# Optimization experiments

Hardware: AMD Instinct MI355X
Metric: run time of the kernel (lower is better)

The kernel has to match this reference:

```python
import jax, jax.numpy as jnp
import numpy as np

B, T, V, H, C = 512, 512, 64, 128, 4


def setup_inputs() -> dict:
    key = jax.random.key(0)
    ks = jax.random.split(key, 32)
    s = 0.05  # weight scale
    inp = {
        'x': jax.random.normal(ks[0], (B, T, V), jnp.float32),
        'd': jax.random.uniform(ks[1], (B, T, 1), jnp.float32),
        'm1': (jax.random.uniform(ks[2], (B, T, V)) < 0.5).astype(jnp.float32),
        'h0_1': 0.1 * jax.random.normal(ks[3], (B, H), jnp.float32),
        'h0_2': 0.1 * jax.random.normal(ks[4], (B, H), jnp.float32),
        'h0_3': 0.1 * jax.random.normal(ks[5], (B, H), jnp.float32),
        'W_ih1': s * jax.random.normal(ks[6], (3 * H, V), jnp.float32),
        'W_hh1': s * jax.random.normal(ks[7], (3 * H, H), jnp.float32),
        'b_ih1': jnp.zeros((3 * H,), jnp.float32),
        'b_hh1': jnp.zeros((3 * H,), jnp.float32),
        'W_ih2': s * jax.random.normal(ks[8], (3 * H, H), jnp.float32),
        'W_hh2': s * jax.random.normal(ks[9], (3 * H, H), jnp.float32),
        'b_ih2': jnp.zeros((3 * H,), jnp.float32),
        'b_hh2': jnp.zeros((3 * H,), jnp.float32),
        'W_ih3': s * jax.random.normal(ks[10], (3 * H, H), jnp.float32),
        'W_hh3': s * jax.random.normal(ks[11], (3 * H, H), jnp.float32),
        'b_ih3': jnp.zeros((3 * H,), jnp.float32),
        'b_hh3': jnp.zeros((3 * H,), jnp.float32),
        'W_out': s * jax.random.normal(ks[12], (C, H), jnp.float32),
        'b_out': jax.random.uniform(ks[13], (C,), jnp.float32),
        'W_dx': s * jax.random.normal(ks[14], (V, 1), jnp.float32),
        'b_dx': jax.random.uniform(ks[15], (V,), jnp.float32),
        'W_dh': s * jax.random.normal(ks[16], (H, 1), jnp.float32),
        'b_dh': jax.random.uniform(ks[17], (H,), jnp.float32),
    }
    return inp


def _gru_cell(xt, h, Wih, Whh, bih, bhh):
    # torch.nn.GRUCell math
    gi = xt @ Wih.T + bih          # [B, 3H]
    gh = h @ Whh.T + bhh           # [B, 3H]
    ir, iz, inn = jnp.split(gi, 3, axis=1)
    hr, hz, hn = jnp.split(gh, 3, axis=1)
    r = jax.nn.sigmoid(ir + hr)
    z = jax.nn.sigmoid(iz + hz)
    n = jnp.tanh(inn + r * hn)
    return (1.0 - z) * n + z * h


def reference(x, d, m1, h0_1, h0_2, h0_3,
              W_ih1, W_hh1, b_ih1, b_hh1,
              W_ih2, W_hh2, b_ih2, b_hh2,
              W_ih3, W_hh3, b_ih3, b_hh3,
              W_out, b_out, W_dx, b_dx, W_dh, b_dh):
    x0 = x[:, 0, :]  # first observation used for imputation

    def head(h):
        return jax.nn.softmax(h @ W_out.T + b_out, axis=1)

    # t = 0: no decay, raw input
    h1 = _gru_cell(x0, h0_1, W_ih1, W_hh1, b_ih1, b_hh1)
    h2 = _gru_cell(h1, h0_2, W_ih2, W_hh2, b_ih2, b_hh2)
    h3 = _gru_cell(h2, h0_3, W_ih3, W_hh3, b_ih3, b_hh3)
    y0 = head(h3)

    # time-major scan inputs for t = 1..T-1
    xs = (jnp.swapaxes(x[:, 1:, :], 0, 1),   # x_t
          jnp.swapaxes(x[:, :-1, :], 0, 1),  # x_{t-1}
          jnp.swapaxes(m1[:, 1:, :], 0, 1),  # m_t
          jnp.swapaxes(d[:, 1:, :], 0, 1))   # d_t [T-1, B, 1]

    def step(carry, inp):
        h1, h2, h3 = carry
        xt, xp, mt, dt = inp
        gamma_h = jnp.exp(-jax.nn.relu(dt @ W_dh.T + b_dh))  # [B, H]
        h1 = h1 * gamma_h
        h2 = h2 * gamma_h
        h3 = h3 * gamma_h
        gamma_x = jnp.exp(-jax.nn.relu(dt @ W_dx.T + b_dx))  # [B, V]
        x1 = (xp * gamma_x + (1.0 - gamma_x) * x0) * (1.0 - mt) + mt * xt
        h1 = _gru_cell(x1, h1, W_ih1, W_hh1, b_ih1, b_hh1)
        h2 = _gru_cell(h1, h2, W_ih2, W_hh2, b_ih2, b_hh2)
        h3 = _gru_cell(h2, h3, W_ih3, W_hh3, b_ih3, b_hh3)
        return (h1, h2, h3), head(h3)

    _, ys = jax.lax.scan(step, (h1, h2, h3), xs)  # [T-1, B, C]
    Y = jnp.concatenate([y0[None], ys], axis=0)    # [T, B, C]
    return jnp.swapaxes(Y, 0, 1)                   # [B, T, C]
```

## Files before the change

### kernel.cpp

```cpp
#include <hip/hip_runtime.h>

#define TT 512
#define VV 64
#define RING 16

typedef _Float16 f16;
typedef f16 f16x8 __attribute__((ext_vector_type(8)));
typedef f16 f16x4 __attribute__((ext_vector_type(4)));
typedef float f32x4v __attribute__((ext_vector_type(4)));
typedef unsigned long long u64;
typedef unsigned u32;

typedef __attribute__((address_space(1))) unsigned gu32;
typedef __attribute__((address_space(1))) unsigned long long gu64;

#define MFMA(A_,B_,C_) __builtin_amdgcn_mfma_f32_16x16x32_f16((A_),(B_),(C_),0,0,0)
#define AT_LD32(p)   __hip_atomic_load((gu32*)(void*)(p), __ATOMIC_RELAXED, __HIP_MEMORY_SCOPE_AGENT)
#define AT_ST32(p,v) __hip_atomic_store((gu32*)(void*)(p),(v), __ATOMIC_RELAXED, __HIP_MEMORY_SCOPE_AGENT)
#define AT_LD64(p)   __hip_atomic_load((gu64*)(void*)(p), __ATOMIC_RELAXED, __HIP_MEMORY_SCOPE_AGENT)
#define AT_ST64(p,v) __hip_atomic_store((gu64*)(void*)(p),(v), __ATOMIC_RELAXED, __HIP_MEMORY_SCOPE_AGENT)

__device__ __forceinline__ void barrier_lds(){ asm volatile("s_waitcnt lgkmcnt(0)\n\ts_barrier" ::: "memory"); }
__device__ __forceinline__ void wait_vm0(){ asm volatile("s_waitcnt vmcnt(0)" ::: "memory"); }
__device__ __forceinline__ float4 ld4(const float* p){ return *(const float4*)p; }

__device__ __forceinline__ f16x8 ldA8(const float* p){
  f16x8 a;
  #pragma unroll
  for (int j = 0; j < 8; ++j) a[j] = (f16)p[j];
  return a;
}

__device__ __forceinline__ int fragOff16(int d0, int b){
  const int kt = d0 >> 5, qq = (d0 >> 3) & 3, j0 = d0 & 7;
  return (kt*64 + qq*16 + b)*8 + j0;
}

__device__ __forceinline__ void fragW_lds(f16x8* buf, int d0, int b, const float* h4){
  f16x4 v;
  #pragma unroll
  for (int e = 0; e < 4; ++e) v[e] = (f16)h4[e];
  *(f16x4*)((f16*)buf + fragOff16(d0, b)) = v;
}

__device__ __forceinline__ void pubFrag(char* slot, int d0, int b, const float* h4){
  union { f16x4 v; u64 u; } uu;
  #pragma unroll
  for (int e = 0; e < 4; ++e) uu.v[e] = (f16)h4[e];
  AT_ST64((u64*)(slot + fragOff16(d0, b)*2), uu.u);
}

__device__ __forceinline__ f16x8 impFrag(const char* slot, int kt, int lane){
  union { u64 u[2]; f16x8 v; } vv;
  const u64* p = (const u64*)(slot + (kt*64 + lane)*16);
  vv.u[0] = AT_LD64((u64*)p);
  vv.u[1] = AT_LD64((u64*)(p + 1));
  return vv.v;
}

__device__ __forceinline__ void spin_ge(u32* f, u32 val){
  if ((threadIdx.x & 63) == 0){
    u32 g = 0;
    while (AT_LD32(f) < val && ++g < (1u << 20)) {}
  }
  asm volatile("" ::: "memory");
}

__device__ __forceinline__ void gates_upd2(const f32x4v& C0, const f32x4v& C1,
                                           const f32x4v& Ci2, const f32x4v& Ch2,
                                           const float* bR, const float* bZ,
                                           const float* bI, const float* bH,
                                           float* hp){
  #pragma unroll
  for (int e = 0; e < 4; ++e){
    float rr = 1.f/(1.f + __expf(-(C0[e] + bR[e])));
    float zz = 1.f/(1.f + __expf(-(C1[e] + bZ[e])));
    float nv = Ci2[e] + bI[e] + rr*(Ch2[e] + bH[e]);
    float nn = 1.f - 2.f/(1.f + __expf(2.f*nv));
    hp[e] = (1.f - zz)*nn + zz*hp[e];
  }
}

__global__ void k_init(u32* wsf){
  const int i = blockIdx.x*256 + threadIdx.x;
  if (i < 4096) AT_ST32(wsf + i, 0u);
}

__launch_bounds__(512, 1)
__global__ void k_pipe(const float* __restrict__ x,   const float* __restrict__ dd,
                       const float* __restrict__ m1,
                       const float* __restrict__ h01, const float* __restrict__ h02,
                       const float* __restrict__ h03,
                       const float* __restrict__ Wih1, const float* __restrict__ Whh1,
                       const float* __restrict__ bih1, const float* __restrict__ bhh1,
                       const float* __restrict__ Wih2, const float* __restrict__ Whh2,
                       const float* __restrict__ bih2, const float* __restrict__ bhh2,
                       const float* __restrict__ Wih3, const float* __restrict__ Whh3,
                       const float* __restrict__ bih3, const float* __restrict__ bhh3,
                       const float* __restrict__ Wout, const float* __restrict__ bout,
                       const float* __restrict__ Wdx,  const float* __restrict__ bdx,
                       const float* __restrict__ Wdh,  const float* __restrict__ bdh,
                       float* __restrict__ y, u32* __restrict__ wsf, char* __restrict__ wsd)
{
  __shared__ f16x8 sW[8*12*64];
  __shared__ f16x8 sFrag[2][256];
  __shared__ f16x8 sX1[2][128];
  __shared__ f16x8 sHead[2][256];

  const int tid = threadIdx.x, wid = tid >> 6, lane = tid & 63;
  const int q = lane >> 4, r = lane & 15;
  const int blk = blockIdx.x, role = blk >> 5, grp = blk & 31, b0 = grp << 4;

  u32* const FL  = wsf;
  u32* const ACK = wsf + 1024;
  u32* const fl0 = FL  + grp*16;
  u32* const ak0 = ACK + grp*16;
  u32* const fl1 = FL  + (32+grp)*16;
  u32* const ak1 = ACK + (32+grp)*16;
  char* const ring0 = wsd + (size_t)grp*RING*4096;
  char* const ring1 = wsd + (size_t)(32+grp)*RING*4096;

  const int dG = wid*16 + 4*q;
  const int wbase = wid*12;

  const float* bihX = (role == 0) ? bih1 : (role == 1) ? bih2 : bih3;
  const float* bhhX = (role == 0) ? bhh1 : (role == 1) ? bhh2 : bhh3;
  const float* h0X  = (role == 0) ? h01  : (role == 1) ? h02  : h03;

  float bR[4], bZ[4], bI[4], bH[4], hS[4], WdhL[4], bdhL[4];
  #pragma unroll
  for (int e = 0; e < 4; ++e){
    const int d = dG + e;
    bR[e] = bihX[d] + bhhX[d];
    bZ[e] = bihX[128+d] + bhhX[128+d];
    bI[e] = bihX[256+d];
    bH[e] = bhhX[256+d];
    WdhL[e] = Wdh[d]; bdhL[e] = bdh[d];
  }
  { float4 a = ld4(h0X + (size_t)(b0+r)*128 + dG); hS[0]=a.x; hS[1]=a.y; hS[2]=a.z; hS[3]=a.w; }
  float dhC = 0.f, dhN = dd[(size_t)(b0+r)*TT + 1];

  if (role == 0){
    f16x8 Ai[3][2];
    #pragma unroll
    for (int g = 0; g < 3; ++g){
      const int mrow = (g*8 + wid)*16 + r;
      #pragma unroll
      for (int kt = 0; kt < 2; ++kt) Ai[g][kt] = ldA8(Wih1 + mrow*64 + kt*32 + q*8);
      #pragma unroll
      for (int kt = 0; kt < 4; ++kt)
        sW[(wbase + g*4 + kt)*64 + lane] = ldA8(Whh1 + mrow*128 + kt*32 + q*8);
    }
    const int bx = (wid & 3)*4 + q, v0 = 4*r;
    float Wdx4[4] = {0,0,0,0}, bdx4[4] = {0,0,0,0};
    float4 xC = {0,0,0,0}, x0v = {0,0,0,0}, xN = {0,0,0,0}, mN = {0,0,0,0};
    float4 xP = {0,0,0,0}, mC = {0,0,0,0};
    float dxC = 0.f, dxN = 0.f;
    if (wid < 4){
      #pragma unroll
      for (int e = 0; e < 4; ++e){ Wdx4[e] = Wdx[v0+e]; bdx4[e] = bdx[v0+e]; }
      xC  = ld4(x + ((size_t)(b0+bx)*TT + 0)*VV + v0);
      x0v = xC;
      xN  = ld4(x  + ((size_t)(b0+bx)*TT + 1)*VV + v0);
      mN  = ld4(m1 + ((size_t)(b0+bx)*TT + 1)*VV + v0);
      dxN = dd[(size_t)(b0+bx)*TT + 1];
      xP = xC; mC = mN; dxC = dxN;
    }
    __syncthreads();

    for (int t = 0; t < TT; ++t){
      const int par = t & 1;
      if ((t & 3) == 0 && t >= 16) spin_ge(ak0, (u32)(t-13));
      if (wid < 4){
        float xi[4];
        if (t == 0){ xi[0]=xC.x; xi[1]=xC.y; xi[2]=xC.z; xi[3]=xC.w; }
        else {
          const float* xc = (const float*)&xC; const float* xp = (const float*)&xP;
          const float* x0e = (const float*)&x0v; const float* me = (const float*)&mC;
          #pragma unroll
          for (int e = 0; e < 4; ++e){
            float gx = __expf(-fmaxf(dxC*Wdx4[e] + bdx4[e], 0.f));
            xi[e] = (xp[e]*gx + (1.f-gx)*x0e[e])*(1.f-me[e]) + me[e]*xc[e];
          }
        }
        fragW_lds(&sX1[par][0], v0, bx, xi);
      }
      if (t >= 1){
        #pragma unroll
        for (int e = 0; e < 4; ++e)
          hS[e] *= __expf(-fmaxf(dhC*WdhL[e] + bdhL[e], 0.f));
      }
      fragW_lds(&sFrag[par][0], dG, r, hS);
      barrier_lds();
      f16x8 bx1[2], bh4[4];
      #pragma unroll
      for (int kt = 0; kt < 2; ++kt) bx1[kt] = sX1[par][kt*64 + lane];
      #pragma unroll
      for (int kt = 0; kt < 4; ++kt) bh4[kt] = sFrag[par][kt*64 + lane];
      f32x4v C0 = {0,0,0,0}, C1 = {0,0,0,0}, Ci2 = {0,0,0,0}, Ch2 = {0,0,0,0};
      #pragma unroll
      for (int kt = 0; kt < 4; ++kt) C0  = MFMA(sW[(wbase + 0*4 + kt)*64 + lane], bh4[kt], C0);
      #pragma unroll
      for (int kt = 0; kt < 4; ++kt) C1  = MFMA(sW[(wbase + 1*4 + kt)*64 + lane], bh4[kt], C1);
      #pragma unroll
      for (int kt = 0; kt < 4; ++kt) Ch2 = MFMA(sW[(wbase + 2*4 + kt)*64 + lane], bh4[kt], Ch2);
      #pragma unroll
      for (int kt = 0; kt < 2; ++kt) C0  = MFMA(Ai[0][kt], bx1[kt], C0);
      #pragma unroll
      for (int kt = 0; kt < 2; ++kt) C1  = MFMA(Ai[1][kt], bx1[kt], C1);
      #pragma unroll
      for (int kt = 0; kt < 2; ++kt) Ci2 = MFMA(Ai[2][kt], bx1[kt], Ci2);
      gates_upd2(C0, C1, Ci2, Ch2, bR, bZ, bI, bH, hS);
      pubFrag(ring0 + (size_t)(t & (RING-1))*4096, dG, r, hS);
      if ((t & 3) == 3){
        wait_vm0();
        barrier_lds();
        if (tid == 0) AT_ST32(fl0, (u32)(t+1));
      }
      dhC = dhN;
      const int tp = (t+2 < TT) ? (t+2) : (TT-1);
      dhN = dd[(size_t)(b0+r)*TT + tp];
      if (wid < 4){
        xP = xC; xC = xN; mC = mN; dxC = dxN;
        xN  = ld4(x  + ((size_t)(b0+bx)*TT + tp)*VV + v0);
        mN  = ld4(m1 + ((size_t)(b0+bx)*TT + tp)*VV + v0);
        dxN = dd[(size_t)(b0+bx)*TT + tp];
      }
    }
    return;
  }

  if (role == 1){
    f16x8 Ah[3][4];
    #pragma unroll
    for (int g = 0; g < 3; ++g){
      const int mrow = (g*8 + wid)*16 + r;
      #pragma unroll
      for (int kt = 0; kt < 4; ++kt){
        sW[(wbase + g*4 + kt)*64 + lane] = ldA8(Wih2 + mrow*128 + kt*32 + q*8);
        Ah[g][kt] = ldA8(Whh2 + mrow*128 + kt*32 + q*8);
      }
    }
    __syncthreads();

    spin_ge(fl0, 8u);
    f16x8 bi[4];
    #pragma unroll
    for (int kt = 0; kt < 4; ++kt) bi[kt] = impFrag(ring0, kt, lane);

    for (int t = 0; t < TT; ++t){
      const int par = t & 1;
      if ((t & 3) == 0 && t >= 16) spin_ge(ak1, (u32)(t-13));
      if (t >= 1){
        #pragma unroll
        for (int e = 0; e < 4; ++e)
          hS[e] *= __expf(-fmaxf(dhC*WdhL[e] + bdhL[e], 0.f));
      }
      fragW_lds(&sFrag[par][0], dG, r, hS);
      barrier_lds();
      if (tid == 0) AT_ST32(ak0, (u32)t);
      f16x8 bh4[4];
      #pragma unroll
      for (int kt = 0; kt < 4; ++kt) bh4[kt] = sFrag[par][kt*64 + lane];
      f32x4v C0 = {0,0,0,0}, C1 = {0,0,0,0}, Ci2 = {0,0,0,0}, Ch2 = {0,0,0,0};
      #pragma unroll
      for (int kt = 0; kt < 4; ++kt) C0  = MFMA(Ah[0][kt], bh4[kt], C0);
      #pragma unroll
      for (int kt = 0; kt < 4; ++kt) C1  = MFMA(Ah[1][kt], bh4[kt], C1);
      #pragma unroll
      for (int kt = 0; kt < 4; ++kt) Ch2 = MFMA(Ah[2][kt], bh4[kt], Ch2);
      #pragma unroll
      for (int kt = 0; kt < 4; ++kt) C0  = MFMA(sW[(wbase + 0*4 + kt)*64 + lane], bi[kt], C0);
      #pragma unroll
      for (int kt = 0; kt < 4; ++kt) C1  = MFMA(sW[(wbase + 1*4 + kt)*64 + lane], bi[kt], C1);
      #pragma unroll
      for (int kt = 0; kt < 4; ++kt) Ci2 = MFMA(sW[(wbase + 2*4 + kt)*64 + lane], bi[kt], Ci2);
      if (t + 1 < TT){
        const char* sIn = ring0 + (size_t)((t+1) & (RING-1))*4096;
        #pragma unroll
        for (int kt = 0; kt < 4; ++kt) bi[kt] = impFrag(sIn, kt, lane);
      }
      gates_upd2(C0, C1, Ci2, Ch2, bR, bZ, bI, bH, hS);
      pubFrag(ring1 + (size_t)(t & (RING-1))*4096, dG, r, hS);
      if ((t & 3) == 3){
        wait_vm0();
        barrier_lds();
        if (tid == 0) AT_ST32(fl1, (u32)(t+1));
        if (t < TT-1) spin_ge(fl0, (u32)(t+7 <= TT ? t+7 : TT));
      }
      dhC = dhN;
      const int tp = (t+2 < TT) ? (t+2) : (TT-1);
      dhN = dd[(size_t)(b0+r)*TT + tp];
    }
    return;
  }

  {
    f16x8 Ah[3][4];
    #pragma unroll
    for (int g = 0; g < 3; ++g){
      const int mrow = (g*8 + wid)*16 + r;
      #pragma unroll
      for (int kt = 0; kt < 4; ++kt){
        sW[(wbase + g*4 + kt)*64 + lane] = ldA8(Wih3 + mrow*128 + kt*32 + q*8);
        Ah[g][kt] = ldA8(Whh3 + mrow*128 + kt*32 + q*8);
      }
    }
    f16x8 aO[4]; float bo4[4] = {0,0,0,0};
    if (wid == 4){
      #pragma unroll
      for (int kt = 0; kt < 4; ++kt){
        f16x8 a;
        #pragma unroll
        for (int j = 0; j < 8; ++j)
          a[j] = (r < 4) ? (f16)Wout[r*128 + kt*32 + q*8 + j] : (f16)0.f;
        aO[kt] = a;
      }
      #pragma unroll
      for (int e = 0; e < 4; ++e) bo4[e] = bout[e];
    }
    __syncthreads();

    spin_ge(fl1, 8u);
    f16x8 bi[4];
    #pragma unroll
    for (int kt = 0; kt < 4; ++kt) bi[kt] = impFrag(ring1, kt, lane);

    for (int s = 0; s <= TT; ++s){
      const int par = s & 1;
      fragW_lds(&sHead[par][0], dG, r, hS);
      if (s < TT){
        if (s >= 1){
          #pragma unroll
          for (int e = 0; e < 4; ++e)
            hS[e] *= __expf(-fmaxf(dhC*WdhL[e] + bdhL[e], 0.f));
        }
        fragW_lds(&sFrag[par][0], dG, r, hS);
      }
      barrier_lds();
      if (s < TT && tid == 0) AT_ST32(ak1, (u32)s);
      if (s < TT){
        f16x8 bh4[4];
        #pragma unroll
        for (int kt = 0; kt < 4; ++kt) bh4[kt] = sFrag[par][kt*64 + lane];
        f32x4v C0 = {0,0,0,0}, C1 = {0,0,0,0}, Ci2 = {0,0,0,0}, Ch2 = {0,0,0,0};
        #pragma unroll
        for (int kt = 0; kt < 4; ++kt) C0  = MFMA(Ah[0][kt], bh4[kt], C0);
        #pragma unroll
        for (int kt = 0; kt < 4; ++kt) C1  = MFMA(Ah[1][kt], bh4[kt], C1);
        #pragma unroll
        for (int kt = 0; kt < 4; ++kt) Ch2 = MFMA(Ah[2][kt], bh4[kt], Ch2);
        #pragma unroll
        for (int kt = 0; kt < 4; ++kt) C0  = MFMA(sW[(wbase + 0*4 + kt)*64 + lane], bi[kt], C0);
        #pragma unroll
        for (int kt = 0; kt < 4; ++kt) C1  = MFMA(sW[(wbase + 1*4 + kt)*64 + lane], bi[kt], C1);
        #pragma unroll
        for (int kt = 0; kt < 4; ++kt) Ci2 = MFMA(sW[(wbase + 2*4 + kt)*64 + lane], bi[kt], Ci2);
        if (s + 1 < TT){
          const char* sIn = ring1 + (size_t)((s+1) & (RING-1))*4096;
          #pragma unroll
          for (int kt = 0; kt < 4; ++kt) bi[kt] = impFrag(sIn, kt, lane);
        }
        gates_upd2(C0, C1, Ci2, Ch2, bR, bZ, bI, bH, hS);
      }
      if (s >= 1 && wid == 4){
        f32x4v cl = {0.f,0.f,0.f,0.f};
        #pragma unroll
        for (int kt = 0; kt < 4; ++kt) cl = MFMA(aO[kt], sHead[par][kt*64 + lane], cl);
        if (lane < 16){
          float l0 = cl[0]+bo4[0], l1 = cl[1]+bo4[1], l2 = cl[2]+bo4[2], l3 = cl[3]+bo4[3];
          float mx = fmaxf(fmaxf(l0,l1), fmaxf(l2,l3));
          float e0 = __expf(l0-mx), e1 = __expf(l1-mx), e2 = __expf(l2-mx), e3 = __expf(l3-mx);
          float inv = 1.f/(e0+e1+e2+e3);
          float4 o; o.x = e0*inv; o.y = e1*inv; o.z = e2*inv; o.w = e3*inv;
          *(float4*)(y + ((size_t)(b0+lane)*TT + (s-1))*4) = o;
        }
      }
      if ((s & 3) == 3 && s < TT-1) spin_ge(fl1, (u32)(s+7 <= TT ? s+7 : TT));
      dhC = dhN;
      const int tp = (s+2 < TT) ? (s+2) : (TT-1);
      dhN = dd[(size_t)(b0+r)*TT + tp];
    }
  }
}

extern "C" void kernel_launch(void* const* d_in, const int* in_sizes, int n_in,
                              void* d_out, int out_size, void* d_ws, size_t ws_size,
                              hipStream_t stream) {
  (void)in_sizes; (void)n_in; (void)out_size; (void)ws_size;
  u32*  wsf = (u32*)d_ws;
  char* wsd = (char*)d_ws + 16384;
  k_init<<<dim3(16), dim3(256), 0, stream>>>(wsf);
  k_pipe<<<dim3(96), dim3(512), 0, stream>>>(
      (const float*)d_in[0],  (const float*)d_in[1],  (const float*)d_in[2],
      (const float*)d_in[3],  (const float*)d_in[4],  (const float*)d_in[5],
      (const float*)d_in[6],  (const float*)d_in[7],  (const float*)d_in[8],  (const float*)d_in[9],
      (const float*)d_in[10], (const float*)d_in[11], (const float*)d_in[12], (const float*)d_in[13],
      (const float*)d_in[14], (const float*)d_in[15], (const float*)d_in[16], (const float*)d_in[17],
      (const float*)d_in[18], (const float*)d_in[19],
      (const float*)d_in[20], (const float*)d_in[21],
      (const float*)d_in[22], (const float*)d_in[23],
      (float*)d_out, wsf, wsd);
}
```

Measured before the change: 1.266 ms.

## Merge GRU layers 2 and 3 into one 1024-thread block with LDS handoff

```diff
diff --git a/kernel.cpp b/kernel.cpp
--- a/kernel.cpp
+++ b/kernel.cpp
@@ -86,7 +86,7 @@
   if (i < 4096) AT_ST32(wsf + i, 0u);
 }
 
-__launch_bounds__(512, 1)
+__launch_bounds__(1024, 1)
 __global__ void k_pipe(const float* __restrict__ x,   const float* __restrict__ dd,
                        const float* __restrict__ m1,
                        const float* __restrict__ h01, const float* __restrict__ h02,
@@ -102,45 +102,30 @@
                        const float* __restrict__ Wdh,  const float* __restrict__ bdh,
                        float* __restrict__ y, u32* __restrict__ wsf, char* __restrict__ wsd)
 {
-  __shared__ f16x8 sW[8*12*64];
-  __shared__ f16x8 sFrag[2][256];
-  __shared__ f16x8 sX1[2][128];
-  __shared__ f16x8 sHead[2][256];
+  __shared__ char smem[131072];
 
   const int tid = threadIdx.x, wid = tid >> 6, lane = tid & 63;
   const int q = lane >> 4, r = lane & 15;
-  const int blk = blockIdx.x, role = blk >> 5, grp = blk & 31, b0 = grp << 4;
-
-  u32* const FL  = wsf;
-  u32* const ACK = wsf + 1024;
-  u32* const fl0 = FL  + grp*16;
-  u32* const ak0 = ACK + grp*16;
-  u32* const fl1 = FL  + (32+grp)*16;
-  u32* const ak1 = ACK + (32+grp)*16;
+  const int blk = blockIdx.x, grp = blk & 31, b0 = grp << 4;
+
+  u32* const fl0 = wsf + grp*16;
+  u32* const ak0 = wsf + 1024 + grp*16;
   char* const ring0 = wsd + (size_t)grp*RING*4096;
-  char* const ring1 = wsd + (size_t)(32+grp)*RING*4096;
-
-  const int dG = wid*16 + 4*q;
-  const int wbase = wid*12;
-
-  const float* bihX = (role == 0) ? bih1 : (role == 1) ? bih2 : bih3;
-  const float* bhhX = (role == 0) ? bhh1 : (role == 1) ? bhh2 : bhh3;
-  const float* h0X  = (role == 0) ? h01  : (role == 1) ? h02  : h03;
-
-  float bR[4], bZ[4], bI[4], bH[4], hS[4], WdhL[4], bdhL[4];
-  #pragma unroll
-  for (int e = 0; e < 4; ++e){
-    const int d = dG + e;
-    bR[e] = bihX[d] + bhhX[d];
-    bZ[e] = bihX[128+d] + bhhX[128+d];
-    bI[e] = bihX[256+d];
-    bH[e] = bhhX[256+d];
-    WdhL[e] = Wdh[d]; bdhL[e] = bdh[d];
-  }
-  { float4 a = ld4(h0X + (size_t)(b0+r)*128 + dG); hS[0]=a.x; hS[1]=a.y; hS[2]=a.z; hS[3]=a.w; }
-  float dhC = 0.f, dhN = dd[(size_t)(b0+r)*TT + 1];
-
-  if (role == 0){
+
+  if (blk < 32){
+    if (wid >= 8){
+      __syncthreads();
+      for (int t = 0; t < TT; ++t){
+        barrier_lds();
+        if ((t & 3) == 3) barrier_lds();
+      }
+      return;
+    }
+    f16x8* const sW     = (f16x8*)smem;
+    f16x8* const sFragP = (f16x8*)(smem + 98304);
+    f16x8* const sX1    = (f16x8*)(smem + 106496);
+
+    const int dG = wid*16 + 4*q;
     f16x8 Ai[3][2];
     #pragma unroll
     for (int g = 0; g < 3; ++g){
@@ -149,8 +134,21 @@
       for (int kt = 0; kt < 2; ++kt) Ai[g][kt] = ldA8(Wih1 + mrow*64 + kt*32 + q*8);
       #pragma unroll
       for (int kt = 0; kt < 4; ++kt)
-        sW[(wbase + g*4 + kt)*64 + lane] = ldA8(Whh1 + mrow*128 + kt*32 + q*8);
-    }
+        sW[(wid*12 + g*4 + kt)*64 + lane] = ldA8(Whh1 + mrow*128 + kt*32 + q*8);
+    }
+    float bR[4], bZ[4], bI[4], bH[4], hS[4], WdhL[4], bdhL[4];
+    #pragma unroll
+    for (int e = 0; e < 4; ++e){
+      const int d = dG + e;
+      bR[e] = bih1[d] + bhh1[d];
+      bZ[e] = bih1[128+d] + bhh1[128+d];
+      bI[e] = bih1[256+d];
+      bH[e] = bhh1[256+d];
+      WdhL[e] = Wdh[d]; bdhL[e] = bdh[d];
+    }
+    { float4 a = ld4(h01 + (size_t)(b0+r)*128 + dG); hS[0]=a.x; hS[1]=a.y; hS[2]=a.z; hS[3]=a.w; }
+    float dhC = 0.f, dhN = dd[(size_t)(b0+r)*TT + 1];
+
     const int bx = (wid & 3)*4 + q, v0 = 4*r;
     float Wdx4[4] = {0,0,0,0}, bdx4[4] = {0,0,0,0};
     float4 xC = {0,0,0,0}, x0v = {0,0,0,0}, xN = {0,0,0,0}, mN = {0,0,0,0};
@@ -183,27 +181,27 @@
             xi[e] = (xp[e]*gx + (1.f-gx)*x0e[e])*(1.f-me[e]) + me[e]*xc[e];
           }
         }
-        fragW_lds(&sX1[par][0], v0, bx, xi);
+        fragW_lds(sX1 + par*128, v0, bx, xi);
       }
       if (t >= 1){
         #pragma unroll
         for (int e = 0; e < 4; ++e)
           hS[e] *= __expf(-fmaxf(dhC*WdhL[e] + bdhL[e], 0.f));
       }
-      fragW_lds(&sFrag[par][0], dG, r, hS);
+      fragW_lds(sFragP + par*256, dG, r, hS);
       barrier_lds();
       f16x8 bx1[2], bh4[4];
       #pragma unroll
-      for (int kt = 0; kt < 2; ++kt) bx1[kt] = sX1[par][kt*64 + lane];
-      #pragma unroll
-      for (int kt = 0; kt < 4; ++kt) bh4[kt] = sFrag[par][kt*64 + lane];
+      for (int kt = 0; kt < 2; ++kt) bx1[kt] = sX1[par*128 + kt*64 + lane];
+      #pragma unroll
+      for (int kt = 0; kt < 4; ++kt) bh4[kt] = sFragP[par*256 + kt*64 + lane];
       f32x4v C0 = {0,0,0,0}, C1 = {0,0,0,0}, Ci2 = {0,0,0,0}, Ch2 = {0,0,0,0};
       #pragma unroll
-      for (int kt = 0; kt < 4; ++kt) C0  = MFMA(sW[(wbase + 0*4 + kt)*64 + lane], bh4[kt], C0);
-      #pragma unroll
-      for (int kt = 0; kt < 4; ++kt) C1  = MFMA(sW[(wbase + 1*4 + kt)*64 + lane], bh4[kt], C1);
-      #pragma unroll
-      for (int kt = 0; kt < 4; ++kt) Ch2 = MFMA(sW[(wbase + 2*4 + kt)*64 + lane], bh4[kt], Ch2);
+      for (int kt = 0; kt < 4; ++kt) C0  = MFMA(sW[(wid*12 + 0*4 + kt)*64 + lane], bh4[kt], C0);
+      #pragma unroll
+      for (int kt = 0; kt < 4; ++kt) C1  = MFMA(sW[(wid*12 + 1*4 + kt)*64 + lane], bh4[kt], C1);
+      #pragma unroll
+      for (int kt = 0; kt < 4; ++kt) Ch2 = MFMA(sW[(wid*12 + 2*4 + kt)*64 + lane], bh4[kt], Ch2);
       #pragma unroll
       for (int kt = 0; kt < 2; ++kt) C0  = MFMA(Ai[0][kt], bx1[kt], C0);
       #pragma unroll
@@ -230,156 +228,167 @@
     return;
   }
 
-  if (role == 1){
-    f16x8 Ah[3][4];
+  {
+    f16x8* const sA  = (f16x8*)smem;
+    f16x8* const sB  = (f16x8*)(smem + 8192);
+    f16x8* const sC  = (f16x8*)(smem + 16384);
+    f16x8* const sD  = (f16x8*)(smem + 24576);
+    f16x8* const sW2 = (f16x8*)(smem + 32768);
+
+    const int half = wid >> 3, w8 = wid & 7;
+    const int dG = w8*16 + 4*q;
+
+    const float* bihX = half ? bih3 : bih2;
+    const float* bhhX = half ? bhh3 : bhh2;
+    const float* h0X  = half ? h03  : h02;
+
+    float bR[4], bZ[4], bI[4], bH[4], hS[4], WdhL[4], bdhL[4];
     #pragma unroll
-    for (int g = 0; g < 3; ++g){
-      const int mrow = (g*8 + wid)*16 + r;
-      #pragma unroll
-      for (int kt = 0; kt < 4; ++kt){
-        sW[(wbase + g*4 + kt)*64 + lane] = ldA8(Wih2 + mrow*128 + kt*32 + q*8);
-        Ah[g][kt] = ldA8(Whh2 + mrow*128 + kt*32 + q*8);
-      }
-    }
-    __syncthreads();
-
-    spin_ge(fl0, 8u);
-    f16x8 bi[4];
-    #pragma unroll
-    for (int kt = 0; kt < 4; ++kt) bi[kt] = impFrag(ring0, kt, lane);
-
-    for (int t = 0; t < TT; ++t){
-      const int par = t & 1;
-      if ((t & 3) == 0 && t >= 16) spin_ge(ak1, (u32)(t-13));
-      if (t >= 1){
+    for (int e = 0; e < 4; ++e){
+      const int d = dG + e;
+      bR[e] = bihX[d] + bhhX[d];
+      bZ[e] = bihX[128+d] + bhhX[128+d];
+      bI[e] = bihX[256+d];
+      bH[e] = bhhX[256+d];
+      WdhL[e] = Wdh[d]; bdhL[e] = bdh[d];
+    }
+    { float4 a = ld4(h0X + (size_t)(b0+r)*128 + dG); hS[0]=a.x; hS[1]=a.y; hS[2]=a.z; hS[3]=a.w; }
+
+    if (half == 0){
+      f16x8 Ah[3][4];
+      #pragma unroll
+      for (int g = 0; g < 3; ++g){
+        const int mrow = (g*8 + w8)*16 + r;
         #pragma unroll
-        for (int e = 0; e < 4; ++e)
-          hS[e] *= __expf(-fmaxf(dhC*WdhL[e] + bdhL[e], 0.f));
-      }
-      fragW_lds(&sFrag[par][0], dG, r, hS);
-      barrier_lds();
-      if (tid == 0) AT_ST32(ak0, (u32)t);
-      f16x8 bh4[4];
-      #pragma unroll
-      for (int kt = 0; kt < 4; ++kt) bh4[kt] = sFrag[par][kt*64 + lane];
-      f32x4v C0 = {0,0,0,0}, C1 = {0,0,0,0}, Ci2 = {0,0,0,0}, Ch2 = {0,0,0,0};
-      #pragma unroll
-      for (int kt = 0; kt < 4; ++kt) C0  = MFMA(Ah[0][kt], bh4[kt], C0);
-      #pragma unroll
-      for (int kt = 0; kt < 4; ++kt) C1  = MFMA(Ah[1][kt], bh4[kt], C1);
-      #pragma unroll
-      for (int kt = 0; kt < 4; ++kt) Ch2 = MFMA(Ah[2][kt], bh4[kt], Ch2);
-      #pragma unroll
-      for (int kt = 0; kt < 4; ++kt) C0  = MFMA(sW[(wbase + 0*4 + kt)*64 + lane], bi[kt], C0);
-      #pragma unroll
-      for (int kt = 0; kt < 4; ++kt) C1  = MFMA(sW[(wbase + 1*4 + kt)*64 + lane], bi[kt], C1);
-      #pragma unroll
-      for (int kt = 0; kt < 4; ++kt) Ci2 = MFMA(sW[(wbase + 2*4 + kt)*64 + lane], bi[kt], Ci2);
-      if (t + 1 < TT){
-        const char* sIn = ring0 + (size_t)((t+1) & (RING-1))*4096;
-        #pragma unroll
-        for (int kt = 0; kt < 4; ++kt) bi[kt] = impFrag(sIn, kt, lane);
-      }
-      gates_upd2(C0, C1, Ci2, Ch2, bR, bZ, bI, bH, hS);
-      pubFrag(ring1 + (size_t)(t & (RING-1))*4096, dG, r, hS);
-      if ((t & 3) == 3){
-        wait_vm0();
-        barrier_lds();
-        if (tid == 0) AT_ST32(fl1, (u32)(t+1));
-        if (t < TT-1) spin_ge(fl0, (u32)(t+7 <= TT ? t+7 : TT));
-      }
-      dhC = dhN;
-      const int tp = (t+2 < TT) ? (t+2) : (TT-1);
-      dhN = dd[(size_t)(b0+r)*TT + tp];
-    }
-    return;
-  }
-
-  {
-    f16x8 Ah[3][4];
-    #pragma unroll
-    for (int g = 0; g < 3; ++g){
-      const int mrow = (g*8 + wid)*16 + r;
-      #pragma unroll
-      for (int kt = 0; kt < 4; ++kt){
-        sW[(wbase + g*4 + kt)*64 + lane] = ldA8(Wih3 + mrow*128 + kt*32 + q*8);
-        Ah[g][kt] = ldA8(Whh3 + mrow*128 + kt*32 + q*8);
-      }
-    }
-    f16x8 aO[4]; float bo4[4] = {0,0,0,0};
-    if (wid == 4){
-      #pragma unroll
-      for (int kt = 0; kt < 4; ++kt){
-        f16x8 a;
-        #pragma unroll
-        for (int j = 0; j < 8; ++j)
-          a[j] = (r < 4) ? (f16)Wout[r*128 + kt*32 + q*8 + j] : (f16)0.f;
-        aO[kt] = a;
-      }
-      #pragma unroll
-      for (int e = 0; e < 4; ++e) bo4[e] = bout[e];
-    }
-    __syncthreads();
-
-    spin_ge(fl1, 8u);
-    f16x8 bi[4];
-    #pragma unroll
-    for (int kt = 0; kt < 4; ++kt) bi[kt] = impFrag(ring1, kt, lane);
-
-    for (int s = 0; s <= TT; ++s){
-      const int par = s & 1;
-      fragW_lds(&sHead[par][0], dG, r, hS);
-      if (s < TT){
-        if (s >= 1){
+        for (int kt = 0; kt < 4; ++kt){
+          sW2[(w8*12 + g*4 + kt)*64 + lane] = ldA8(Wih2 + mrow*128 + kt*32 + q*8);
+          Ah[g][kt] = ldA8(Whh2 + mrow*128 + kt*32 + q*8);
+        }
+      }
+      float dhC = 0.f, dhN = dd[(size_t)(b0+r)*TT + 1];
+      __syncthreads();
+
+      spin_ge(fl0, 8u);
+      f16x8 bi[4];
+      #pragma unroll
+      for (int kt = 0; kt < 4; ++kt) bi[kt] = impFrag(ring0, kt, lane);
+
+      for (int s = 0; s <= TT+1; ++s){
+        const int par = s & 1;
+        if (s <= TT) fragW_lds(sB + par*256, dG, r, hS);
+        if (s >= 1 && s < TT){
           #pragma unroll
           for (int e = 0; e < 4; ++e)
             hS[e] *= __expf(-fmaxf(dhC*WdhL[e] + bdhL[e], 0.f));
         }
-        fragW_lds(&sFrag[par][0], dG, r, hS);
-      }
-      barrier_lds();
-      if (s < TT && tid == 0) AT_ST32(ak1, (u32)s);
-      if (s < TT){
-        f16x8 bh4[4];
+        if (s < TT) fragW_lds(sA + par*256, dG, r, hS);
+        barrier_lds();
+        if (s < TT){
+          if (tid == 0) AT_ST32(ak0, (u32)s);
+          f16x8 bh4[4];
+          #pragma unroll
+          for (int kt = 0; kt < 4; ++kt) bh4[kt] = sA[par*256 + kt*64 + lane];
+          f32x4v C0 = {0,0,0,0}, C1 = {0,0,0,0}, Ci2 = {0,0,0,0}, Ch2 = {0,0,0,0};
+          #pragma unroll
+          for (int kt = 0; kt < 4; ++kt) C0  = MFMA(Ah[0][kt], bh4[kt], C0);
+          #pragma unroll
+          for (int kt = 0; kt < 4; ++kt) C1  = MFMA(Ah[1][kt], bh4[kt], C1);
+          #pragma unroll
+          for (int kt = 0; kt < 4; ++kt) Ch2 = MFMA(Ah[2][kt], bh4[kt], Ch2);
+          #pragma unroll
+          for (int kt = 0; kt < 4; ++kt) C0  = MFMA(sW2[(w8*12 + 0*4 + kt)*64 + lane], bi[kt], C0);
+          #pragma unroll
+          for (int kt = 0; kt < 4; ++kt) C1  = MFMA(sW2[(w8*12 + 1*4 + kt)*64 + lane], bi[kt], C1);
+          #pragma unroll
+          for (int kt = 0; kt < 4; ++kt) Ci2 = MFMA(sW2[(w8*12 + 2*4 + kt)*64 + lane], bi[kt], Ci2);
+          if (s + 1 < TT){
+            const char* sIn = ring0 + (size_t)((s+1) & (RING-1))*4096;
+            #pragma unroll
+            for (int kt = 0; kt < 4; ++kt) bi[kt] = impFrag(sIn, kt, lane);
+          }
+          gates_upd2(C0, C1, Ci2, Ch2, bR, bZ, bI, bH, hS);
+          if ((s & 3) == 3 && s < TT-1) spin_ge(fl0, (u32)(s+7 <= TT ? s+7 : TT));
+        }
+        dhC = dhN;
+        const int tp = (s+2 < TT) ? (s+2) : (TT-1);
+        dhN = dd[(size_t)(b0+r)*TT + tp];
+      }
+    } else {
+      f16x8 Ai3[3][4], Ah3[3][4];
+      #pragma unroll
+      for (int g = 0; g < 3; ++g){
+        const int mrow = (g*8 + w8)*16 + r;
         #pragma unroll
-        for (int kt = 0; kt < 4; ++kt) bh4[kt] = sFrag[par][kt*64 + lane];
-        f32x4v C0 = {0,0,0,0}, C1 = {0,0,0,0}, Ci2 = {0,0,0,0}, Ch2 = {0,0,0,0};
+        for (int kt = 0; kt < 4; ++kt){
+          Ai3[g][kt] = ldA8(Wih3 + mrow*128 + kt*32 + q*8);
+          Ah3[g][kt] = ldA8(Whh3 + mrow*128 + kt*32 + q*8);
+        }
+      }
+      f16x8 aO[4]; float bo4[4] = {0,0,0,0};
+      if (wid == 8){
         #pragma unroll
-        for (int kt = 0; kt < 4; ++kt) C0  = MFMA(Ah[0][kt], bh4[kt], C0);
+        for (int kt = 0; kt < 4; ++kt){
+          f16x8 a;
+          #pragma unroll
+          for (int j = 0; j < 8; ++j)
+            a[j] = (r < 4) ? (f16)Wout[r*128 + kt*32 + q*8 + j] : (f16)0.f;
+          aO[kt] = a;
+        }
         #pragma unroll
-        for (int kt = 0; kt < 4; ++kt) C1  = MFMA(Ah[1][kt], bh4[kt], C1);
-        #pragma unroll
-        for (int kt = 0; kt < 4; ++kt) Ch2 = MFMA(Ah[2][kt], bh4[kt], Ch2);
-        #pragma unroll
-        for (int kt = 0; kt < 4; ++kt) C0  = MFMA(sW[(wbase + 0*4 + kt)*64 + lane], bi[kt], C0);
-        #pragma unroll
-        for (int kt = 0; kt < 4; ++kt) C1  = MFMA(sW[(wbase + 1*4 + kt)*64 + lane], bi[kt], C1);
-        #pragma unroll
-        for (int kt = 0; kt < 4; ++kt) Ci2 = MFMA(sW[(wbase + 2*4 + kt)*64 + lane], bi[kt], Ci2);
-        if (s + 1 < TT){
-          const char* sIn = ring1 + (size_t)((s+1) & (RING-1))*4096;
-          #pragma unroll
-          for (int kt = 0; kt < 4; ++kt) bi[kt] = impFrag(sIn, kt, lane);
-        }
-        gates_upd2(C0, C1, Ci2, Ch2, bR, bZ, bI, bH, hS);
-      }
-      if (s >= 1 && wid == 4){
-        f32x4v cl = {0.f,0.f,0.f,0.f};
-        #pragma unroll
-        for (int kt = 0; kt < 4; ++kt) cl = MFMA(aO[kt], sHead[par][kt*64 + lane], cl);
-        if (lane < 16){
-          float l0 = cl[0]+bo4[0], l1 = cl[1]+bo4[1], l2 = cl[2]+bo4[2], l3 = cl[3]+bo4[3];
-          float mx = fmaxf(fmaxf(l0,l1), fmaxf(l2,l3));
-          float e0 = __expf(l0-mx), e1 = __expf(l1-mx), e2 = __expf(l2-mx), e3 = __expf(l3-mx);
-          float inv = 1.f/(e0+e1+e2+e3);
-          float4 o; o.x = e0*inv; o.y = e1*inv; o.z = e2*inv; o.w = e3*inv;
-          *(float4*)(y + ((size_t)(b0+lane)*TT + (s-1))*4) = o;
-        }
-      }
-      if ((s & 3) == 3 && s < TT-1) spin_ge(fl1, (u32)(s+7 <= TT ? s+7 : TT));
-      dhC = dhN;
-      const int tp = (s+2 < TT) ? (s+2) : (TT-1);
-      dhN = dd[(size_t)(b0+r)*TT + tp];
+        for (int e = 0; e < 4; ++e) bo4[e] = bout[e];
+      }
+      float dhC = 0.f, dhN = dd[(size_t)(b0+r)*TT + 0];
+      __syncthreads();
+
+      for (int s = 0; s <= TT+1; ++s){
+        const int par = s & 1;
+        fragW_lds(sD + par*256, dG, r, hS);
+        if (s >= 2 && s <= TT){
+          #pragma unroll
+          for (int e = 0; e < 4; ++e)
+            hS[e] *= __expf(-fmaxf(dhC*WdhL[e] + bdhL[e], 0.f));
+        }
+        if (s >= 1 && s <= TT) fragW_lds(sC + par*256, dG, r, hS);
+        barrier_lds();
+        if (s >= 1 && s <= TT){
+          f16x8 bh4[4], bi3[4];
+          #pragma unroll
+          for (int kt = 0; kt < 4; ++kt) bh4[kt] = sC[par*256 + kt*64 + lane];
+          #pragma unroll
+          for (int kt = 0; kt < 4; ++kt) bi3[kt] = sB[par*256 + kt*64 + lane];
+          f32x4v C0 = {0,0,0,0}, C1 = {0,0,0,0}, Ci2 = {0,0,0,0}, Ch2 = {0,0,0,0};
+          #pragma unroll
+          for (int kt = 0; kt < 4; ++kt) C0  = MFMA(Ah3[0][kt], bh4[kt], C0);
+          #pragma unroll
+          for (int kt = 0; kt < 4; ++kt) C1  = MFMA(Ah3[1][kt], bh4[kt], C1);
+          #pragma unroll
+          for (int kt = 0; kt < 4; ++kt) Ch2 = MFMA(Ah3[2][kt], bh4[kt], Ch2);
+          #pragma unroll
+          for (int kt = 0; kt < 4; ++kt) C0  = MFMA(Ai3[0][kt], bi3[kt], C0);
+          #pragma unroll
+          for (int kt = 0; kt < 4; ++kt) C1  = MFMA(Ai3[1][kt], bi3[kt], C1);
+          #pragma unroll
+          for (int kt = 0; kt < 4; ++kt) Ci2 = MFMA(Ai3[2][kt], bi3[kt], Ci2);
+          gates_upd2(C0, C1, Ci2, Ch2, bR, bZ, bI, bH, hS);
+        }
+        if (s >= 2 && wid == 8){
+          f32x4v cl = {0.f,0.f,0.f,0.f};
+          #pragma unroll
+          for (int kt = 0; kt < 4; ++kt) cl = MFMA(aO[kt], sD[par*256 + kt*64 + lane], cl);
+          if (lane < 16){
+            float l0 = cl[0]+bo4[0], l1 = cl[1]+bo4[1], l2 = cl[2]+bo4[2], l3 = cl[3]+bo4[3];
+            float mx = fmaxf(fmaxf(l0,l1), fmaxf(l2,l3));
+            float e0 = __expf(l0-mx), e1 = __expf(l1-mx), e2 = __expf(l2-mx), e3 = __expf(l3-mx);
+            float inv = 1.f/(e0+e1+e2+e3);
+            float4 o; o.x = e0*inv; o.y = e1*inv; o.z = e2*inv; o.w = e3*inv;
+            *(float4*)(y + ((size_t)(b0+lane)*TT + (s-2))*4) = o;
+          }
+        }
+        dhC = dhN;
+        const int tn = s + 1;
+        const int tp = (tn < TT) ? tn : (TT-1);
+        dhN = dd[(size_t)(b0+r)*TT + tp];
+      }
     }
   }
 }
@@ -391,7 +400,7 @@
   u32*  wsf = (u32*)d_ws;
   char* wsd = (char*)d_ws + 16384;
   k_init<<<dim3(16), dim3(256), 0, stream>>>(wsf);
-  k_pipe<<<dim3(96), dim3(512), 0, stream>>>(
+  k_pipe<<<dim3(64), dim3(1024), 0, stream>>>(
       (const float*)d_in[0],  (const float*)d_in[1],  (const float*)d_in[2],
       (const float*)d_in[3],  (const float*)d_in[4],  (const float*)d_in[5],
       (const float*)d_in[6],  (const float*)d_in[7],  (const float*)d_in[8],  (const float*)d_in[9],
```

Measured after the change: 2.718 ms. 2.15x slower.

## Hoist input-side MFMAs off the recurrent critical path and coarsen inter-layer sync

Applied to the files above, without the earlier changes.

```diff
diff --git a/kernel.cpp b/kernel.cpp
--- a/kernel.cpp
+++ b/kernel.cpp
@@ -2,7 +2,7 @@
 
 #define TT 512
 #define VV 64
-#define RING 16
+#define RING 32
 
 typedef _Float16 f16;
 typedef f16 f16x8 __attribute__((ext_vector_type(8)));
@@ -111,12 +111,10 @@
   const int q = lane >> 4, r = lane & 15;
   const int blk = blockIdx.x, role = blk >> 5, grp = blk & 31, b0 = grp << 4;
 
-  u32* const FL  = wsf;
-  u32* const ACK = wsf + 1024;
-  u32* const fl0 = FL  + grp*16;
-  u32* const ak0 = ACK + grp*16;
-  u32* const fl1 = FL  + (32+grp)*16;
-  u32* const ak1 = ACK + (32+grp)*16;
+  u32* const fl0 = wsf + grp*16;
+  u32* const ak0 = wsf + 1024 + grp*16;
+  u32* const fl1 = wsf + (32+grp)*16;
+  u32* const ak1 = wsf + 1024 + (32+grp)*16;
   char* const ring0 = wsd + (size_t)grp*RING*4096;
   char* const ring1 = wsd + (size_t)(32+grp)*RING*4096;
 
@@ -154,8 +152,7 @@
     const int bx = (wid & 3)*4 + q, v0 = 4*r;
     float Wdx4[4] = {0,0,0,0}, bdx4[4] = {0,0,0,0};
     float4 xC = {0,0,0,0}, x0v = {0,0,0,0}, xN = {0,0,0,0}, mN = {0,0,0,0};
-    float4 xP = {0,0,0,0}, mC = {0,0,0,0};
-    float dxC = 0.f, dxN = 0.f;
+    float dxN = 0.f;
     if (wid < 4){
       #pragma unroll
       for (int e = 0; e < 4; ++e){ Wdx4[e] = Wdx[v0+e]; bdx4[e] = bdx[v0+e]; }
@@ -164,26 +161,36 @@
       xN  = ld4(x  + ((size_t)(b0+bx)*TT + 1)*VV + v0);
       mN  = ld4(m1 + ((size_t)(b0+bx)*TT + 1)*VV + v0);
       dxN = dd[(size_t)(b0+bx)*TT + 1];
-      xP = xC; mC = mN; dxC = dxN;
+      float xi0[4] = {xC.x, xC.y, xC.z, xC.w};
+      fragW_lds(&sX1[0][0], v0, bx, xi0);
     }
     __syncthreads();
 
     for (int t = 0; t < TT; ++t){
       const int par = t & 1;
-      if ((t & 3) == 0 && t >= 16) spin_ge(ak0, (u32)(t-13));
-      if (wid < 4){
+      if ((t & 7) == 0 && t >= 32) spin_ge(ak0, (u32)(t-24));
+      if (wid < 4 && t + 1 < TT){
         float xi[4];
-        if (t == 0){ xi[0]=xC.x; xi[1]=xC.y; xi[2]=xC.z; xi[3]=xC.w; }
-        else {
-          const float* xc = (const float*)&xC; const float* xp = (const float*)&xP;
-          const float* x0e = (const float*)&x0v; const float* me = (const float*)&mC;
-          #pragma unroll
-          for (int e = 0; e < 4; ++e){
-            float gx = __expf(-fmaxf(dxC*Wdx4[e] + bdx4[e], 0.f));
-            xi[e] = (xp[e]*gx + (1.f-gx)*x0e[e])*(1.f-me[e]) + me[e]*xc[e];
-          }
+        const float* xc = (const float*)&xN; const float* xp = (const float*)&xC;
+        const float* x0e = (const float*)&x0v; const float* me = (const float*)&mN;
+        #pragma unroll
+        for (int e = 0; e < 4; ++e){
+          float gx = __expf(-fmaxf(dxN*Wdx4[e] + bdx4[e], 0.f));
+          xi[e] = (xp[e]*gx + (1.f-gx)*x0e[e])*(1.f-me[e]) + me[e]*xc[e];
         }
-        fragW_lds(&sX1[par][0], v0, bx, xi);
+        fragW_lds(&sX1[(t+1)&1][0], v0, bx, xi);
+      }
+      f32x4v C0 = {0,0,0,0}, C1 = {0,0,0,0}, Ci2 = {0,0,0,0}, Ch2 = {0,0,0,0};
+      {
+        f16x8 bx1[2];
+        #pragma unroll
+        for (int kt = 0; kt < 2; ++kt) bx1[kt] = sX1[par][kt*64 + lane];
+        #pragma unroll
+        for (int kt = 0; kt < 2; ++kt) C0  = MFMA(Ai[0][kt], bx1[kt], C0);
+        #pragma unroll
+        for (int kt = 0; kt < 2; ++kt) C1  = MFMA(Ai[1][kt], bx1[kt], C1);
+        #pragma unroll
+        for (int kt = 0; kt < 2; ++kt) Ci2 = MFMA(Ai[2][kt], bx1[kt], Ci2);
       }
       if (t >= 1){
         #pragma unroll
@@ -192,27 +199,18 @@
       }
       fragW_lds(&sFrag[par][0], dG, r, hS);
       barrier_lds();
-      f16x8 bx1[2], bh4[4];
-      #pragma unroll
-      for (int kt = 0; kt < 2; ++kt) bx1[kt] = sX1[par][kt*64 + lane];
+      f16x8 bh4[4];
       #pragma unroll
       for (int kt = 0; kt < 4; ++kt) bh4[kt] = sFrag[par][kt*64 + lane];
-      f32x4v C0 = {0,0,0,0}, C1 = {0,0,0,0}, Ci2 = {0,0,0,0}, Ch2 = {0,0,0,0};
       #pragma unroll
       for (int kt = 0; kt < 4; ++kt) C0  = MFMA(sW[(wbase + 0*4 + kt)*64 + lane], bh4[kt], C0);
       #pragma unroll
       for (int kt = 0; kt < 4; ++kt) C1  = MFMA(sW[(wbase + 1*4 + kt)*64 + lane], bh4[kt], C1);
       #pragma unroll
       for (int kt = 0; kt < 4; ++kt) Ch2 = MFMA(sW[(wbase + 2*4 + kt)*64 + lane], bh4[kt], Ch2);
-      #pragma unroll
-      for (int kt = 0; kt < 2; ++kt) C0  = MFMA(Ai[0][kt], bx1[kt], C0);
-      #pragma unroll
-      for (int kt = 0; kt < 2; ++kt) C1  = MFMA(Ai[1][kt], bx1[kt], C1);
-      #pragma unroll
-      for (int kt = 0; kt < 2; ++kt) Ci2 = MFMA(Ai[2][kt], bx1[kt], Ci2);
       gates_upd2(C0, C1, Ci2, Ch2, bR, bZ, bI, bH, hS);
       pubFrag(ring0 + (size_t)(t & (RING-1))*4096, dG, r, hS);
-      if ((t & 3) == 3){
+      if ((t & 7) == 7){
         wait_vm0();
         barrier_lds();
         if (tid == 0) AT_ST32(fl0, (u32)(t+1));
@@ -221,7 +219,7 @@
       const int tp = (t+2 < TT) ? (t+2) : (TT-1);
       dhN = dd[(size_t)(b0+r)*TT + tp];
       if (wid < 4){
-        xP = xC; xC = xN; mC = mN; dxC = dxN;
+        xC = xN;
         xN  = ld4(x  + ((size_t)(b0+bx)*TT + tp)*VV + v0);
         mN  = ld4(m1 + ((size_t)(b0+bx)*TT + tp)*VV + v0);
         dxN = dd[(size_t)(b0+bx)*TT + tp];
@@ -250,25 +248,8 @@
 
     for (int t = 0; t < TT; ++t){
       const int par = t & 1;
-      if ((t & 3) == 0 && t >= 16) spin_ge(ak1, (u32)(t-13));
-      if (t >= 1){
-        #pragma unroll
-        for (int e = 0; e < 4; ++e)
-          hS[e] *= __expf(-fmaxf(dhC*WdhL[e] + bdhL[e], 0.f));
-      }
-      fragW_lds(&sFrag[par][0], dG, r, hS);
-      barrier_lds();
-      if (tid == 0) AT_ST32(ak0, (u32)t);
-      f16x8 bh4[4];
-      #pragma unroll
-      for (int kt = 0; kt < 4; ++kt) bh4[kt] = sFrag[par][kt*64 + lane];
+      if ((t & 7) == 0 && t >= 32) spin_ge(ak1, (u32)(t-24));
       f32x4v C0 = {0,0,0,0}, C1 = {0,0,0,0}, Ci2 = {0,0,0,0}, Ch2 = {0,0,0,0};
-      #pragma unroll
-      for (int kt = 0; kt < 4; ++kt) C0  = MFMA(Ah[0][kt], bh4[kt], C0);
-      #pragma unroll
-      for (int kt = 0; kt < 4; ++kt) C1  = MFMA(Ah[1][kt], bh4[kt], C1);
-      #pragma unroll
-      for (int kt = 0; kt < 4; ++kt) Ch2 = MFMA(Ah[2][kt], bh4[kt], Ch2);
       #pragma unroll
       for (int kt = 0; kt < 4; ++kt) C0  = MFMA(sW[(wbase + 0*4 + kt)*64 + lane], bi[kt], C0);
       #pragma unroll
@@ -280,13 +261,29 @@
         #pragma unroll
         for (int kt = 0; kt < 4; ++kt) bi[kt] = impFrag(sIn, kt, lane);
       }
+      if (t >= 1){
+        #pragma unroll
+        for (int e = 0; e < 4; ++e)
+          hS[e] *= __expf(-fmaxf(dhC*WdhL[e] + bdhL[e], 0.f));
+      }
+      fragW_lds(&sFrag[par][0], dG, r, hS);
+      barrier_lds();
+      f16x8 bh4[4];
+      #pragma unroll
+      for (int kt = 0; kt < 4; ++kt) bh4[kt] = sFrag[par][kt*64 + lane];
+      #pragma unroll
+      for (int kt = 0; kt < 4; ++kt) C0  = MFMA(Ah[0][kt], bh4[kt], C0);
+      #pragma unroll
+      for (int kt = 0; kt < 4; ++kt) C1  = MFMA(Ah[1][kt], bh4[kt], C1);
+      #pragma unroll
+      for (int kt = 0; kt < 4; ++kt) Ch2 = MFMA(Ah[2][kt], bh4[kt], Ch2);
       gates_upd2(C0, C1, Ci2, Ch2, bR, bZ, bI, bH, hS);
       pubFrag(ring1 + (size_t)(t & (RING-1))*4096, dG, r, hS);
-      if ((t & 3) == 3){
+      if ((t & 7) == 7){
         wait_vm0();
         barrier_lds();
-        if (tid == 0) AT_ST32(fl1, (u32)(t+1));
-        if (t < TT-1) spin_ge(fl0, (u32)(t+7 <= TT ? t+7 : TT));
+        if (tid == 0){ AT_ST32(fl1, (u32)(t+1)); AT_ST32(ak0, (u32)(t+1)); }
+        if (t < TT-1) spin_ge(fl0, (u32)(t+9 <= TT ? t+9 : TT));
       }
       dhC = dhN;
       const int tp = (t+2 < TT) ? (t+2) : (TT-1);
@@ -329,7 +326,19 @@
     for (int s = 0; s <= TT; ++s){
       const int par = s & 1;
       fragW_lds(&sHead[par][0], dG, r, hS);
+      f32x4v C0 = {0,0,0,0}, C1 = {0,0,0,0}, Ci2 = {0,0,0,0}, Ch2 = {0,0,0,0};
       if (s < TT){
+        #pragma unroll
+        for (int kt = 0; kt < 4; ++kt) C0  = MFMA(sW[(wbase + 0*4 + kt)*64 + lane], bi[kt], C0);
+        #pragma unroll
+        for (int kt = 0; kt < 4; ++kt) C1  = MFMA(sW[(wbase + 1*4 + kt)*64 + lane], bi[kt], C1);
+        #pragma unroll
+        for (int kt = 0; kt < 4; ++kt) Ci2 = MFMA(sW[(wbase + 2*4 + kt)*64 + lane], bi[kt], Ci2);
+        if (s + 1 < TT){
+          const char* sIn = ring1 + (size_t)((s+1) & (RING-1))*4096;
+          #pragma unroll
+          for (int kt = 0; kt < 4; ++kt) bi[kt] = impFrag(sIn, kt, lane);
+        }
         if (s >= 1){
           #pragma unroll
           for (int e = 0; e < 4; ++e)
@@ -338,29 +347,16 @@
         fragW_lds(&sFrag[par][0], dG, r, hS);
       }
       barrier_lds();
-      if (s < TT && tid == 0) AT_ST32(ak1, (u32)s);
       if (s < TT){
         f16x8 bh4[4];
         #pragma unroll
         for (int kt = 0; kt < 4; ++kt) bh4[kt] = sFrag[par][kt*64 + lane];
-        f32x4v C0 = {0,0,0,0}, C1 = {0,0,0,0}, Ci2 = {0,0,0,0}, Ch2 = {0,0,0,0};
         #pragma unroll
         for (int kt = 0; kt < 4; ++kt) C0  = MFMA(Ah[0][kt], bh4[kt], C0);
         #pragma unroll
         for (int kt = 0; kt < 4; ++kt) C1  = MFMA(Ah[1][kt], bh4[kt], C1);
         #pragma unroll
         for (int kt = 0; kt < 4; ++kt) Ch2 = MFMA(Ah[2][kt], bh4[kt], Ch2);
-        #pragma unroll
-        for (int kt = 0; kt < 4; ++kt) C0  = MFMA(sW[(wbase + 0*4 + kt)*64 + lane], bi[kt], C0);
-        #pragma unroll
-        for (int kt = 0; kt < 4; ++kt) C1  = MFMA(sW[(wbase + 1*4 + kt)*64 + lane], bi[kt], C1);
-        #pragma unroll
-        for (int kt = 0; kt < 4; ++kt) Ci2 = MFMA(sW[(wbase + 2*4 + kt)*64 + lane], bi[kt], Ci2);
-        if (s + 1 < TT){
-          const char* sIn = ring1 + (size_t)((s+1) & (RING-1))*4096;
-          #pragma unroll
-          for (int kt = 0; kt < 4; ++kt) bi[kt] = impFrag(sIn, kt, lane);
-        }
         gates_upd2(C0, C1, Ci2, Ch2, bR, bZ, bI, bH, hS);
       }
       if (s >= 1 && wid == 4){
@@ -376,7 +372,10 @@
           *(float4*)(y + ((size_t)(b0+lane)*TT + (s-1))*4) = o;
         }
       }
-      if ((s & 3) == 3 && s < TT-1) spin_ge(fl1, (u32)(s+7 <= TT ? s+7 : TT));
+      if ((s & 7) == 7 && s < TT){
+        if (tid == 0) AT_ST32(ak1, (u32)(s+1));
+        if (s < TT-1) spin_ge(fl1, (u32)(s+9 <= TT ? s+9 : TT));
+      }
       dhC = dhN;
       const int tp = (s+2 < TT) ? (s+2) : (TT-1);
       dhN = dd[(size_t)(b0+r)*TT + tp];
```

Result: faster. 1.175 ms (-7.1%).
